# Optimization experiments

Hardware: AMD Instinct MI355X
Metric: run time of the kernel (lower is better)

## Reference

```python
import jax, jax.numpy as jnp
import numpy as np


def setup_inputs() -> dict:
    key = jax.random.key(0)
    inputs = jax.random.normal(key, (4, 1024, 64), dtype=jnp.float32)
    return {"inputs": inputs}


def reference(inputs):
    # inputs: (B, N, D)
    # scores[b,i,j] = sum_d tanh(x[b,i,d] + x[b,j,d])
    addition = inputs[:, :, None, :] + inputs[:, None, :, :]  # (B, N, N, D)
    e_values = jnp.tanh(addition).sum(axis=-1)                # (B, N, N)
    weights = jax.nn.softmax(e_values, axis=-1)               # (B, N, N)
    out = jnp.einsum("bij,bjd->bid", weights, inputs)         # (B, N, D)
    return out
```

## Files before the change

kernel.cpp:

```cpp
#include <hip/hip_runtime.h>


#define NB 4
#define NN 1024
#define ND 64
#define TJ 64
#define TI 4
#define NTILES (NN / TJ)

#if __has_builtin(__builtin_amdgcn_exp2f)
#define EXP2F(x) __builtin_amdgcn_exp2f(x)
#else
#define EXP2F(x) exp2f(x)
#endif
#if __has_builtin(__builtin_amdgcn_rcpf)
#define RCPF(x) __builtin_amdgcn_rcpf(x)
#else
#define RCPF(x) (1.0f / (x))
#endif

static constexpr float C_SCALE = 2.8853900817779268f;
static constexpr float K_SHIFT = 46.166241308446828f;

typedef float v2f __attribute__((ext_vector_type(2)));

#define PKFMA(a, b, c) __builtin_elementwise_fma((a), (b), (c))

__device__ __forceinline__ v2f vlo(float4 v) { v2f r; r.x = v.x; r.y = v.y; return r; }
__device__ __forceinline__ v2f vhi(float4 v) { v2f r; r.x = v.z; r.y = v.w; return r; }

__global__ __launch_bounds__(256) void prep_kernel(const float* __restrict__ x,
                                                   float* __restrict__ E) {
    int idx = blockIdx.x * 256 + threadIdx.x;
    float4 v = ((const float4*)x)[idx];
    float4 e;
    e.x = EXP2F(C_SCALE * v.x);
    e.y = EXP2F(C_SCALE * v.y);
    e.z = EXP2F(C_SCALE * v.z);
    e.w = EXP2F(C_SCALE * v.w);
    ((float4*)E)[idx] = e;
}

template <bool HAS_E>
__global__ __launch_bounds__(256, 3) void addattn_kernel(const float* __restrict__ x,
                                                         const float* __restrict__ E,
                                                         float* __restrict__ out) {
    __shared__ float E_lds[TJ * ND];
    __shared__ float x_lds[TJ * ND];

    const int tid   = threadIdx.x;
    const int lane  = tid & 63;
    const int wave  = tid >> 6;
    const int wg    = blockIdx.x;
    const int b     = wg >> 8;
    const int ibase = (wg & 255) * TI;
    const int i0    = __builtin_amdgcn_readfirstlane(ibase + wave);

    const float* xb  = x + (size_t)b * NN * ND;
    const float* Eb  = E + (size_t)b * NN * ND;
    const float* Eip = Eb + (size_t)i0 * ND;

    v2f ei2[32];
    if (!HAS_E) {
        #pragma unroll
        for (int c = 0; c < 16; ++c) {
            float4 xiq = *(const float4*)&xb[(size_t)i0 * ND + c * 4];
            v2f lo, hi;
            lo.x = EXP2F(C_SCALE * xiq.x);
            lo.y = EXP2F(C_SCALE * xiq.y);
            hi.x = EXP2F(C_SCALE * xiq.z);
            hi.y = EXP2F(C_SCALE * xiq.w);
            ei2[2 * c] = lo;
            ei2[2 * c + 1] = hi;
        }
    }

    v2f acc2[32];
    #pragma unroll
    for (int k = 0; k < 32; ++k) acc2[k] = (v2f){0.f, 0.f};
    float dn = 0.f;

    for (int t = 0; t < NTILES; ++t) {
        __syncthreads();
        {
            const float4* srcx = (const float4*)(xb + (size_t)t * TJ * ND);
            const float4* srcE = (const float4*)(Eb + (size_t)t * TJ * ND);
            #pragma unroll
            for (int it = 0; it < (TJ * ND / 4) / 256; ++it) {
                int idx = it * 256 + tid;
                int j   = idx >> 4;
                int c   = idx & 15;
                int w   = j * ND + ((c ^ (j & 15)) << 2);
                float4 xv = srcx[idx];
                *(float4*)&x_lds[w] = xv;
                float4 ev;
                if (HAS_E) {
                    ev = srcE[idx];
                } else {
                    ev.x = EXP2F(C_SCALE * xv.x);
                    ev.y = EXP2F(C_SCALE * xv.y);
                    ev.z = EXP2F(C_SCALE * xv.z);
                    ev.w = EXP2F(C_SCALE * xv.w);
                }
                *(float4*)&E_lds[w] = ev;
            }
        }
        __syncthreads();

        const int key = lane & 15;
        v2f rse = {0.f, 0.f}, rso = {0.f, 0.f};
        #pragma unroll
        for (int c = 0; c < 16; ++c) {
            float4 ejq = *(const float4*)&E_lds[lane * ND + ((c ^ key) << 2)];
            v2f eil, eih;
            if (HAS_E) {
                float4 eiq = *(const float4*)&Eip[c * 4];
                eil = vlo(eiq); eih = vhi(eiq);
            } else {
                eil = ei2[2 * c]; eih = ei2[2 * c + 1];
            }
            v2f a = eil * vlo(ejq);
            v2f q = eih * vhi(ejq);
            v2f p = a + q;
            v2f r = PKFMA(a, q, p + 1.0f);
            v2f tt; tt.x = RCPF(r.x); tt.y = RCPF(r.y);
            if (c & 1) rso = PKFMA(p + 2.0f, tt, rso);
            else       rse = PKFMA(p + 2.0f, tt, rse);
        }
        v2f rs = rse + rso;
        float rsum = rs.x + rs.y;
        float w = EXP2F(fmaf(-C_SCALE, rsum, K_SHIFT));
        dn += w;
        v2f w2; w2.x = w; w2.y = w;

        #pragma unroll
        for (int c = 0; c < 16; ++c) {
            float4 xq = *(const float4*)&x_lds[lane * ND + ((c ^ key) << 2)];
            acc2[2 * c]     = PKFMA(w2, vlo(xq), acc2[2 * c]);
            acc2[2 * c + 1] = PKFMA(w2, vhi(xq), acc2[2 * c + 1]);
        }
    }

    float* accf = (float*)acc2;
    #pragma unroll
    for (int s = 0; s < 6; ++s) {
        const int half = 32 >> s;
        const int sel  = (lane >> (5 - s)) & 1;
        #pragma unroll
        for (int k = 0; k < half; ++k) {
            float keep = sel ? accf[k + half] : accf[k];
            float send = sel ? accf[k] : accf[k + half];
            float recv = __shfl_xor(send, half, 64);
            accf[k] = keep + recv;
        }
    }
    #pragma unroll
    for (int s = 0; s < 6; ++s) dn += __shfl_xor(dn, 1 << s, 64);

    out[((size_t)b * NN + i0) * ND + lane] = accf[0] * RCPF(dn);
}

extern "C" void kernel_launch(void* const* d_in, const int* in_sizes, int n_in,
                              void* d_out, int out_size, void* d_ws, size_t ws_size,
                              hipStream_t stream) {
    const float* x = (const float*)d_in[0];
    float* out = (float*)d_out;
    const size_t e_bytes = (size_t)NB * NN * ND * sizeof(float);

    dim3 grid(NB * (NN / TI));
    dim3 block(256);

    if (ws_size >= e_bytes) {
        float* E = (float*)d_ws;
        prep_kernel<<<dim3(NB * NN * ND / 4 / 256), dim3(256), 0, stream>>>(x, E);
        addattn_kernel<true><<<grid, block, 0, stream>>>(x, E, out);
    } else {
        addattn_kernel<false><<<grid, block, 0, stream>>>(x, (const float*)nullptr, out);
    }
}
```

Measured before the change: 65.24 us.

## Prefetch next j-tile into registers while computing current tile

Global loads of the next x and E tile are issued into registers before the current tile's compute. They are written to LDS after the compute, between two barriers, so global memory latency overlaps with the tanh and accumulate math. This costs 32 extra VGPRs for the staging registers, which could reduce occupancy under launch_bounds(256,3) or cause spills.

Result: slower. 118.1 us (+80.9%).

```diff
diff --git a/kernel.cpp b/kernel.cpp
--- a/kernel.cpp
+++ b/kernel.cpp
@@ -60,6 +60,18 @@
     const float* Eb  = E + (size_t)b * NN * ND;
     const float* Eip = Eb + (size_t)i0 * ND;
 
+    float4 px[4], pE[4];
+    {
+        const float4* srcx = (const float4*)xb;
+        const float4* srcE = (const float4*)Eb;
+        #pragma unroll
+        for (int it = 0; it < 4; ++it) {
+            int idx = it * 256 + tid;
+            px[it] = srcx[idx];
+            if (HAS_E) pE[it] = srcE[idx];
+        }
+    }
+
     v2f ei2[32];
     if (!HAS_E) {
         #pragma unroll
@@ -75,37 +87,42 @@
         }
     }
 
+    #pragma unroll
+    for (int it = 0; it < 4; ++it) {
+        int idx = it * 256 + tid;
+        int j   = idx >> 4;
+        int c   = idx & 15;
+        int wof = j * ND + ((c ^ (j & 15)) << 2);
+        *(float4*)&x_lds[wof] = px[it];
+        float4 ev;
+        if (HAS_E) {
+            ev = pE[it];
+        } else {
+            ev.x = EXP2F(C_SCALE * px[it].x);
+            ev.y = EXP2F(C_SCALE * px[it].y);
+            ev.z = EXP2F(C_SCALE * px[it].z);
+            ev.w = EXP2F(C_SCALE * px[it].w);
+        }
+        *(float4*)&E_lds[wof] = ev;
+    }
+    __syncthreads();
+
     v2f acc2[32];
     #pragma unroll
     for (int k = 0; k < 32; ++k) acc2[k] = (v2f){0.f, 0.f};
     float dn = 0.f;
 
     for (int t = 0; t < NTILES; ++t) {
-        __syncthreads();
-        {
-            const float4* srcx = (const float4*)(xb + (size_t)t * TJ * ND);
-            const float4* srcE = (const float4*)(Eb + (size_t)t * TJ * ND);
+        if (t + 1 < NTILES) {
+            const float4* srcx = (const float4*)(xb + (size_t)(t + 1) * TJ * ND);
+            const float4* srcE = (const float4*)(Eb + (size_t)(t + 1) * TJ * ND);
             #pragma unroll
-            for (int it = 0; it < (TJ * ND / 4) / 256; ++it) {
+            for (int it = 0; it < 4; ++it) {
                 int idx = it * 256 + tid;
-                int j   = idx >> 4;
-                int c   = idx & 15;
-                int w   = j * ND + ((c ^ (j & 15)) << 2);
-                float4 xv = srcx[idx];
-                *(float4*)&x_lds[w] = xv;
-                float4 ev;
-                if (HAS_E) {
-                    ev = srcE[idx];
-                } else {
-                    ev.x = EXP2F(C_SCALE * xv.x);
-                    ev.y = EXP2F(C_SCALE * xv.y);
-                    ev.z = EXP2F(C_SCALE * xv.z);
-                    ev.w = EXP2F(C_SCALE * xv.w);
-                }
-                *(float4*)&E_lds[w] = ev;
+                px[it] = srcx[idx];
+                if (HAS_E) pE[it] = srcE[idx];
             }
         }
-        __syncthreads();
 
         const int key = lane & 15;
         v2f rse = {0.f, 0.f}, rso = {0.f, 0.f};
@@ -128,8 +145,7 @@
             else       rse = PKFMA(p + 2.0f, tt, rse);
         }
         v2f rs = rse + rso;
-        float rsum = rs.x + rs.y;
-        float w = EXP2F(fmaf(-C_SCALE, rsum, K_SHIFT));
+        float w = EXP2F(fmaf(-C_SCALE, rs.x + rs.y, K_SHIFT));
         dn += w;
         v2f w2; w2.x = w; w2.y = w;
 
@@ -138,6 +154,29 @@
             float4 xq = *(const float4*)&x_lds[lane * ND + ((c ^ key) << 2)];
             acc2[2 * c]     = PKFMA(w2, vlo(xq), acc2[2 * c]);
             acc2[2 * c + 1] = PKFMA(w2, vhi(xq), acc2[2 * c + 1]);
+        }
+
+        if (t + 1 < NTILES) {
+            __syncthreads();
+            #pragma unroll
+            for (int it = 0; it < 4; ++it) {
+                int idx = it * 256 + tid;
+                int j   = idx >> 4;
+                int c   = idx & 15;
+                int wof = j * ND + ((c ^ (j & 15)) << 2);
+                *(float4*)&x_lds[wof] = px[it];
+                float4 ev;
+                if (HAS_E) {
+                    ev = pE[it];
+                } else {
+                    ev.x = EXP2F(C_SCALE * px[it].x);
+                    ev.y = EXP2F(C_SCALE * px[it].y);
+                    ev.z = EXP2F(C_SCALE * px[it].z);
+                    ev.w = EXP2F(C_SCALE * px[it].w);
+                }
+                *(float4*)&E_lds[wof] = ev;
+            }
+            __syncthreads();
         }
     }
 
```
